# Kernel optimization log

Hardware: AMD Instinct MI355X
Metric: run time of the kernel (lower is better)

The kernel has to match this reference:

```python
import jax, jax.numpy as jnp
import numpy as np

D_MODEL = 1024
N_HEADS = 16
HEAD_DIM = D_MODEL // N_HEADS
D_FF = 4096
B, S = 2, 2048


def layer_norm(x, gamma, beta, eps=1e-5):
    mu = jnp.mean(x, axis=-1, keepdims=True)
    var = jnp.mean(jnp.square(x - mu), axis=-1, keepdims=True)
    return (x - mu) * jax.lax.rsqrt(var + eps) * gamma + beta


def setup_inputs() -> dict:
    key = jax.random.key(0)
    ks = jax.random.split(key, 8)
    s = 0.02
    return {
        "x": jax.random.normal(ks[0], (B, S, D_MODEL), dtype=jnp.float32),
        "qkv_w": jax.random.normal(ks[1], (D_MODEL, 3 * D_MODEL), dtype=jnp.float32) * s,
        "qkv_b": jnp.zeros((3 * D_MODEL,), jnp.float32),
        "out_w": jax.random.normal(ks[2], (D_MODEL, D_MODEL), dtype=jnp.float32) * s,
        "out_b": jnp.zeros((D_MODEL,), jnp.float32),
        "attn_ln_g": jnp.ones((D_MODEL,), jnp.float32),
        "attn_ln_b": jnp.zeros((D_MODEL,), jnp.float32),
        "norm1_g": jnp.ones((D_MODEL,), jnp.float32),
        "norm1_b": jnp.zeros((D_MODEL,), jnp.float32),
        "ff_ln_g": jnp.ones((D_MODEL,), jnp.float32),
        "ff_ln_b": jnp.zeros((D_MODEL,), jnp.float32),
        "w1": jax.random.normal(ks[3], (D_MODEL, D_FF), dtype=jnp.float32) * s,
        "b1": jnp.zeros((D_FF,), jnp.float32),
        "w2": jax.random.normal(ks[4], (D_FF, D_MODEL), dtype=jnp.float32) * s,
        "b2": jnp.zeros((D_MODEL,), jnp.float32),
        "norm2_g": jnp.ones((D_MODEL,), jnp.float32),
        "norm2_b": jnp.zeros((D_MODEL,), jnp.float32),
    }


def reference(x, qkv_w, qkv_b, out_w, out_b, attn_ln_g, attn_ln_b,
              norm1_g, norm1_b, ff_ln_g, ff_ln_b, w1, b1, w2, b2,
              norm2_g, norm2_b):
    # --- MultiHeadAttention (pre-LN inside the attn block) ---
    h = layer_norm(x, attn_ln_g, attn_ln_b)
    qkv = h @ qkv_w + qkv_b                       # [B,S,3D]
    qkv = qkv.reshape(B, S, 3, N_HEADS, HEAD_DIM)
    q = jnp.transpose(qkv[:, :, 0], (0, 2, 1, 3))  # [B,H,S,hd]
    k = jnp.transpose(qkv[:, :, 1], (0, 2, 1, 3))
    v = jnp.transpose(qkv[:, :, 2], (0, 2, 1, 3))
    scale = HEAD_DIM ** -0.5
    scores = jnp.einsum("bhqd,bhkd->bhqk", q, k) * scale  # [B,H,S,S]
    attn = jax.nn.softmax(scores, axis=-1)
    ctx = jnp.einsum("bhqk,bhkd->bhqd", attn, v)
    ctx = jnp.transpose(ctx, (0, 2, 1, 3)).reshape(B, S, D_MODEL)
    attn_out = ctx @ out_w + out_b

    # residual + post-LN
    x = layer_norm(x + attn_out, norm1_g, norm1_b)

    # --- FeedForward (pre-LN inside the FF block, GELU) ---
    h = layer_norm(x, ff_ln_g, ff_ln_b)
    ff = jax.nn.gelu(h @ w1 + b1, approximate=False) @ w2 + b2

    # residual + post-LN
    return layer_norm(x + ff, norm2_g, norm2_b)
```

## Files before the change

kernel.cpp:

```cpp
#include <hip/hip_runtime.h>
#include <hip/hip_bf16.h>

typedef __attribute__((ext_vector_type(4))) float f32x4;
typedef __attribute__((ext_vector_type(16))) float f32x16;
typedef __attribute__((ext_vector_type(8))) short s16x8;
typedef __attribute__((ext_vector_type(4))) short s16x4;

#define DM 1024
#define NH 16
#define NB 2
#define NS 2048
#define NTOK (NB*NS)

__device__ __forceinline__ float b2f(short u){
  union { unsigned int i; float f; } c; c.i = ((unsigned int)(unsigned short)u) << 16; return c.f;
}
__device__ __forceinline__ short f2b(float f){
  __hip_bfloat16 h = __float2bfloat16(f);
  return __builtin_bit_cast(short, h);
}
__device__ __forceinline__ void gload16(const void* g, void* l){
  __builtin_amdgcn_global_load_lds((const __attribute__((address_space(1))) void*)g,
                                   (__attribute__((address_space(3))) void*)l, 16, 0, 0);
}
__device__ __forceinline__ s16x4 tr16(const void* p){
  s16x4 r;
  asm volatile("ds_read_b64_tr_b16 %0, %1"
               : "=v"(r)
               : "v"((const __attribute__((address_space(3))) short*)p)
               : "memory");
  return r;
}

#define BARX { __builtin_amdgcn_sched_barrier(0); __builtin_amdgcn_s_barrier(); __builtin_amdgcn_sched_barrier(0); }
#define LGK  { asm volatile("s_waitcnt lgkmcnt(0)" ::: "memory"); __builtin_amdgcn_sched_barrier(0); }

template<int MIH>
__device__ __forceinline__ void rdA(s16x8 (&Af)[4][2], const short* Ab, int foff){
  #pragma unroll
  for (int m=0;m<4;m++)
    #pragma unroll
    for (int ks=0;ks<2;ks++)
      Af[m][ks] = *(const s16x8*)(Ab + (MIH*4+m)*1024 + ks*512 + foff);
}
template<int NIH>
__device__ __forceinline__ void rdB(s16x8 (&Bf)[4][2], const short* Bb, int foff){
  #pragma unroll
  for (int n=0;n<2;n++)
    #pragma unroll
    for (int ks=0;ks<2;ks++)
      Bf[NIH*2+n][ks] = *(const s16x8*)(Bb + (NIH*2+n)*1024 + ks*512 + foff);
}
template<int MIH,int NIH>
__device__ __forceinline__ void mmQ(f32x4 (&acc)[8][4], s16x8 (&Af)[4][2], s16x8 (&Bf)[4][2]){
  __builtin_amdgcn_s_setprio(1);
  #pragma unroll
  for (int m=0;m<4;m++)
    #pragma unroll
    for (int n=0;n<2;n++)
      #pragma unroll
      for (int ks=0;ks<2;ks++)
        acc[MIH*4+m][NIH*2+n] = __builtin_amdgcn_mfma_f32_16x16x32_bf16(
            Af[m][ks], Bf[NIH*2+n][ks], acc[MIH*4+m][NIH*2+n], 0,0,0);
  __builtin_amdgcn_s_setprio(0);
}

template<int GELU, int SPLITS>
__global__ __launch_bounds__(512,2) void gemm8p(
    const short* __restrict__ A, const short* __restrict__ Bt,
    const float* __restrict__ bias,
    short* __restrict__ C0, short* __restrict__ C1,
    short* __restrict__ C2, short* __restrict__ C3,
    int M, int N, int Ktot)
{
  __shared__ short Al[2*16384];
  __shared__ short Bl[2*16384];
  int tid = threadIdx.x, wid = tid>>6, lane = tid&63;
  int la = lane&15, lb = lane>>4;
  int z = blockIdx.z;
  const int Ksp = Ktot / SPLITS;
  short* C = (SPLITS==1) ? C0 : (z==0?C0 : z==1?C1 : z==2?C2 : C3);
  const short* Az  = A  + z*Ksp;
  const short* Btz = Bt + z*Ksp;
  int nbn = N>>8;
  int nwg = (M>>8)*nbn;
  int bid = (int)blockIdx.x;
  int sid = (bid&7)*(nwg>>3) + (bid>>3);
  int bm = sid / nbn, bn = sid % nbn;
  int wm2 = wid>>2, wn4 = wid&3;
  int bhalf = wn4>>1, bq4 = (wn4&1)*4;

  const short* aA0 = Az  + (size_t)(bm*256)*Ktot;
  const short* aA1 = Az  + (size_t)(bm*256+128)*Ktot;
  const short* bB0 = Btz + (size_t)(bn*256)*Ktot;
  const short* bB1 = Btz + (size_t)(bn*256+128)*Ktot;

  auto stG = [&](short* dstHalf, const short* srcRow0, int kt){
    #pragma unroll
    for (int c=0;c<2;c++){
      int s = c*8 + wid;
      int row = ((s>>1)<<4) + (lane>>2);
      int kk  = kt + ((s&1)<<5) + (((lane&3)<<3) ^ ((lane&32)>>1));
      gload16(srcRow0 + (size_t)row*Ktot + kk, dstHalf + s*512);
    }
  };

  int NJ = Ksp>>7;
  stG(&Al[0], aA0, 0);      stG(&Al[8192], aA1, 0);
  stG(&Bl[0], bB0, 0);      stG(&Bl[8192], bB1, 0);
  stG(&Bl[16384], bB0, 64); stG(&Bl[16384+8192], bB1, 64);
  asm volatile("s_waitcnt vmcnt(4)" ::: "memory");
  BARX;

  f32x4 acc[8][4] = {};
  s16x8 Af[4][2], Bf[4][2];
  int foff = la*32 + ((lb*8) ^ ((la&8)<<1));

  const short* Ab0c = &Al[wm2*8192];
  const short* Ab1c = &Al[16384 + wm2*8192];
  const short* Bb0c = &Bl[bhalf*8192 + bq4*1024];
  const short* Bb1c = &Bl[16384 + bhalf*8192 + bq4*1024];

  for (int j=0;j<NJ;j++){
    bool more = (j+1 < NJ);
    int ktA  = (2*j+1)*64;
    int ktN0 = (2*j+2)*64, ktN1 = (2*j+3)*64;
    rdA<0>(Af, Ab0c, foff); rdB<0>(Bf, Bb0c, foff);
    stG(&Al[16384], aA0, ktA);
    BARX; LGK; mmQ<0,0>(acc,Af,Bf); BARX;
    rdB<1>(Bf, Bb0c, foff);
    stG(&Al[16384+8192], aA1, ktA);
    BARX; LGK; mmQ<0,1>(acc,Af,Bf); BARX;
    rdA<1>(Af, Ab0c, foff);
    if (more) stG(&Bl[0], bB0, ktN0);
    BARX; LGK; mmQ<1,1>(acc,Af,Bf); BARX;
    if (more){ stG(&Bl[8192], bB1, ktN0);
               asm volatile("s_waitcnt vmcnt(4)" ::: "memory"); }
    else     { asm volatile("s_waitcnt vmcnt(0)" ::: "memory"); }
    BARX; mmQ<1,0>(acc,Af,Bf); BARX;
    rdA<0>(Af, Ab1c, foff); rdB<0>(Bf, Bb1c, foff);
    if (more) stG(&Al[0], aA0, ktN0);
    BARX; LGK; mmQ<0,0>(acc,Af,Bf); BARX;
    rdB<1>(Bf, Bb1c, foff);
    if (more) stG(&Al[8192], aA1, ktN0);
    BARX; LGK; mmQ<0,1>(acc,Af,Bf); BARX;
    rdA<1>(Af, Ab1c, foff);
    if (more) stG(&Bl[16384], bB0, ktN1);
    BARX; LGK; mmQ<1,1>(acc,Af,Bf); BARX;
    if (more){ stG(&Bl[16384+8192], bB1, ktN1);
               asm volatile("s_waitcnt vmcnt(4)" ::: "memory"); }
    else     { asm volatile("s_waitcnt vmcnt(0)" ::: "memory"); }
    BARX; mmQ<1,0>(acc,Af,Bf); BARX;
  }

  #pragma unroll
  for (int ni=0;ni<4;ni++){
    int col = bn*256 + wn4*64 + ni*16 + la;
    float bv = (SPLITS==1 || z==0) ? bias[col] : 0.0f;
    #pragma unroll
    for (int mi=0;mi<8;mi++){
      int row0 = bm*256 + wm2*128 + mi*16 + lb*4;
      #pragma unroll
      for (int j=0;j<4;j++){
        float v = acc[mi][ni][j] + bv;
        if (GELU) v = 0.5f*v*(1.0f + erff(v*0.70710678118f));
        C[(size_t)(row0+j)*N + col] = f2b(v);
      }
    }
  }
}

__global__ __launch_bounds__(512,1) void attn_fwd(const short* __restrict__ qkv, short* __restrict__ ctx)
{
  __shared__ short KlS[2*4096];
  __shared__ short VlS[2*4096];
  __shared__ float stats[8*32];
  char* Kl = (char*)KlS; char* Vl = (char*)VlS;
  int tid=threadIdx.x, w=tid>>6, lane=tid&63;
  int q5=lane&31, hi=lane>>5, la=lane&15, lb0=(lane>>4)&1;
  int qt=blockIdx.x, bh=blockIdx.y;
  int b=bh>>4, h=bh&15;
  int q0w = qt*256 + w*32;

  const short* qp = qkv + (size_t)(b*NS+q0w+q5)*3072 + h*64 + hi*8;
  s16x8 qf[4];
  #pragma unroll
  for (int ds=0; ds<4; ds++){
    s16x8 v = *(const s16x8*)(qp + ds*16);
    #pragma unroll
    for (int j=0;j<8;j++) v[j] = f2b(b2f(v[j])*0.125f);
    qf[ds]=v;
  }

  int krow = 8*w + (lane>>3);
  int kcolS = (((lane&7) ^ ((lane>>3)&7)) << 3);
  const short* Ksrc = qkv + (size_t)(b*NS+krow)*3072 + h*64 + 1024 + kcolS;
  int vk = 16*(w&3) + 8*hi + 4*lb0 + ((lane>>1)&3);
  int vd = 32*(w>>2) + 16*((lane>>3)&1) + 8*(lane&1);
  const short* Vsrc = qkv + (size_t)(b*NS+vk)*3072 + h*64 + 2048 + vd;

  int sw = (q5&7)<<4;
  int baseK = q5*128 + ((hi<<4) ^ (sw&16)) + (sw&96);
  int baseV = hi*512 + lb0*128 + la*8;

  f32x16 cacc0={}, cacc1={};
  float mrow=-1e30f, lrow=0.f;
  const size_t tstep = (size_t)64*3072;

  gload16(Ksrc, Kl + w*1024);
  gload16(Vsrc, Vl + w*1024);
  __syncthreads();
  int cur=0;

  for (int t=0;t<NS/64;t++){
    if (t+1 < NS/64){
      gload16(Ksrc + (size_t)(t+1)*tstep, Kl + (cur^1)*8192 + w*1024);
      gload16(Vsrc + (size_t)(t+1)*tstep, Vl + (cur^1)*8192 + w*1024);
    }
    const char* Kb = Kl + cur*8192;
    f32x16 s0={}, s1={};
    #pragma unroll
    for (int ds=0; ds<4; ds++){
      s16x8 k0 = *(const s16x8*)(Kb + (baseK ^ (ds<<5)));
      s16x8 k1 = *(const s16x8*)(Kb + 4096 + (baseK ^ (ds<<5)));
      s0 = __builtin_amdgcn_mfma_f32_32x32x16_bf16(k0, qf[ds], s0, 0,0,0);
      s1 = __builtin_amdgcn_mfma_f32_32x32x16_bf16(k1, qf[ds], s1, 0,0,0);
    }
    float pmax = s0[0];
    #pragma unroll
    for (int r=1;r<16;r++) pmax = fmaxf(pmax, s0[r]);
    #pragma unroll
    for (int r=0;r<16;r++) pmax = fmaxf(pmax, s1[r]);
    pmax = fmaxf(pmax, __shfl_xor(pmax, 32, 64));
    if (__any(pmax > mrow + 8.f)){
      float mnew = fmaxf(mrow, pmax);
      float corr = __expf(mrow - mnew);
      if (!hi) stats[w*32+q5] = corr;
      LGK;
      lrow *= corr; mrow = mnew;
      #pragma unroll
      for (int r=0;r<16;r++){
        float c = stats[w*32 + ((r&3)+8*(r>>2)+4*hi)];
        cacc0[r]*=c; cacc1[r]*=c;
      }
    }
    float rs = 0.f;
    #pragma unroll
    for (int r=0;r<16;r++){ float p=__expf(s0[r]-mrow); s0[r]=p; rs+=p; }
    #pragma unroll
    for (int r=0;r<16;r++){ float p=__expf(s1[r]-mrow); s1[r]=p; rs+=p; }
    rs += __shfl_xor(rs, 32, 64);
    lrow += rs;
    unsigned int D0[4][2], D1[4][2], R0[4][2], R1[4][2];
    #pragma unroll
    for (int bb=0;bb<4;bb++)
      #pragma unroll
      for (int hh=0;hh<2;hh++){
        D0[bb][hh] = (unsigned int)(unsigned short)f2b(s0[4*bb+2*hh]) |
                     ((unsigned int)(unsigned short)f2b(s0[4*bb+2*hh+1])<<16);
        D1[bb][hh] = (unsigned int)(unsigned short)f2b(s1[4*bb+2*hh]) |
                     ((unsigned int)(unsigned short)f2b(s1[4*bb+2*hh+1])<<16);
      }
    #pragma unroll
    for (int bb=0;bb<4;bb++)
      #pragma unroll
      for (int hh=0;hh<2;hh++){
        R0[bb][hh] = (unsigned int)__shfl_xor((int)D0[bb][hh], 32, 64);
        R1[bb][hh] = (unsigned int)__shfl_xor((int)D1[bb][hh], 32, 64);
      }
    union PA { unsigned int u[4]; s16x8 v; } pa[4];
    #pragma unroll
    for (int e=0;e<2;e++)
      #pragma unroll
      for (int hh=0;hh<2;hh++){
        pa[e].u[hh]     = hi ? R0[2*e+1][hh] : D0[2*e][hh];
        pa[e].u[2+hh]   = hi ? D0[2*e+1][hh] : R0[2*e][hh];
        pa[2+e].u[hh]   = hi ? R1[2*e+1][hh] : D1[2*e][hh];
        pa[2+e].u[2+hh] = hi ? D1[2*e+1][hh] : R1[2*e][hh];
      }
    const char* Vb = Vl + cur*8192;
    #pragma unroll
    for (int ks=0;ks<4;ks++){
      s16x4 t00 = tr16(Vb + ks*1024 +        0 + baseV);
      s16x4 t01 = tr16(Vb + ks*1024 +      256 + baseV);
      s16x4 t10 = tr16(Vb + ks*1024 + 4096     + baseV);
      s16x4 t11 = tr16(Vb + ks*1024 + 4096+256 + baseV);
      LGK;
      union { s16x4 hh[2]; s16x8 v; } u0, u1;
      u0.hh[0]=t00; u0.hh[1]=t01;
      u1.hh[0]=t10; u1.hh[1]=t11;
      cacc0 = __builtin_amdgcn_mfma_f32_32x32x16_bf16(pa[ks].v, u0.v, cacc0, 0,0,0);
      cacc1 = __builtin_amdgcn_mfma_f32_32x32x16_bf16(pa[ks].v, u1.v, cacc1, 0,0,0);
    }
    __syncthreads();
    cur ^= 1;
  }
  if (!hi) stats[w*32+q5] = 1.0f/lrow;
  LGK;
  #pragma unroll
  for (int r=0;r<16;r++){
    int q = (r&3)+8*(r>>2)+4*hi;
    float linv = stats[w*32+q];
    size_t row = (size_t)(b*NS + q0w + q)*DM + h*64;
    ctx[row + q5]      = f2b(cacc0[r]*linv);
    ctx[row + 32 + q5] = f2b(cacc1[r]*linv);
  }
}

__device__ __forceinline__ void wred2(float& s, float& ss){
  #pragma unroll
  for (int m=1;m<64;m<<=1){ s += __shfl_xor(s,m,64); ss += __shfl_xor(ss,m,64); }
}

__global__ __launch_bounds__(256) void ln_in(const float* __restrict__ x,
    const float* __restrict__ g, const float* __restrict__ be, short* __restrict__ out)
{
  int row=blockIdx.x, tid=threadIdx.x;
  __shared__ float r1[4], r2[4];
  float4 v = ((const float4*)(x + (size_t)row*DM))[tid];
  float s=v.x+v.y+v.z+v.w, ss=v.x*v.x+v.y*v.y+v.z*v.z+v.w*v.w;
  wred2(s,ss);
  if ((tid&63)==0){ r1[tid>>6]=s; r2[tid>>6]=ss; }
  __syncthreads();
  s=r1[0]+r1[1]+r1[2]+r1[3]; ss=r2[0]+r2[1]+r2[2]+r2[3];
  float mu=s*(1.f/DM);
  float rstd=rsqrtf(ss*(1.f/DM)-mu*mu+1e-5f);
  float4 gv=((const float4*)g)[tid], bv=((const float4*)be)[tid];
  s16x4 o;
  o[0]=f2b((v.x-mu)*rstd*gv.x+bv.x);
  o[1]=f2b((v.y-mu)*rstd*gv.y+bv.y);
  o[2]=f2b((v.z-mu)*rstd*gv.z+bv.z);
  o[3]=f2b((v.w-mu)*rstd*gv.w+bv.w);
  *(s16x4*)(out + (size_t)row*DM + tid*4) = o;
}

__global__ __launch_bounds__(256) void ln_chain(const float* __restrict__ x,
    const short* __restrict__ p0, const short* __restrict__ p1,
    const short* __restrict__ p2, const short* __restrict__ p3,
    const float* __restrict__ g1, const float* __restrict__ be1,
    const float* __restrict__ g2, const float* __restrict__ be2,
    float* __restrict__ x1, short* __restrict__ h2)
{
  int row=blockIdx.x, tid=threadIdx.x;
  __shared__ float r1[4], r2[4], r3[4], r4[4];
  size_t off = (size_t)row*DM + tid*4;
  float4 xv = ((const float4*)(x + (size_t)row*DM))[tid];
  s16x4 a0=*(const s16x4*)(p0+off), a1=*(const s16x4*)(p1+off);
  s16x4 a2=*(const s16x4*)(p2+off), a3=*(const s16x4*)(p3+off);
  float4 y;
  y.x = xv.x + b2f(a0[0])+b2f(a1[0])+b2f(a2[0])+b2f(a3[0]);
  y.y = xv.y + b2f(a0[1])+b2f(a1[1])+b2f(a2[1])+b2f(a3[1]);
  y.z = xv.z + b2f(a0[2])+b2f(a1[2])+b2f(a2[2])+b2f(a3[2]);
  y.w = xv.w + b2f(a0[3])+b2f(a1[3])+b2f(a2[3])+b2f(a3[3]);
  float s=y.x+y.y+y.z+y.w, ss=y.x*y.x+y.y*y.y+y.z*y.z+y.w*y.w;
  wred2(s,ss);
  if ((tid&63)==0){ r1[tid>>6]=s; r2[tid>>6]=ss; }
  __syncthreads();
  s=r1[0]+r1[1]+r1[2]+r1[3]; ss=r2[0]+r2[1]+r2[2]+r2[3];
  float mu=s*(1.f/DM);
  float rstd=rsqrtf(ss*(1.f/DM)-mu*mu+1e-5f);
  float4 g1v=((const float4*)g1)[tid], b1v=((const float4*)be1)[tid];
  float4 xo;
  xo.x=(y.x-mu)*rstd*g1v.x+b1v.x;
  xo.y=(y.y-mu)*rstd*g1v.y+b1v.y;
  xo.z=(y.z-mu)*rstd*g1v.z+b1v.z;
  xo.w=(y.w-mu)*rstd*g1v.w+b1v.w;
  ((float4*)(x1 + (size_t)row*DM))[tid] = xo;
  float s2=xo.x+xo.y+xo.z+xo.w, ss2=xo.x*xo.x+xo.y*xo.y+xo.z*xo.z+xo.w*xo.w;
  wred2(s2,ss2);
  if ((tid&63)==0){ r3[tid>>6]=s2; r4[tid>>6]=ss2; }
  __syncthreads();
  s2=r3[0]+r3[1]+r3[2]+r3[3]; ss2=r4[0]+r4[1]+r4[2]+r4[3];
  float mu2=s2*(1.f/DM);
  float rstd2=rsqrtf(ss2*(1.f/DM)-mu2*mu2+1e-5f);
  float4 g2v=((const float4*)g2)[tid], b2v=((const float4*)be2)[tid];
  s16x4 o;
  o[0]=f2b((xo.x-mu2)*rstd2*g2v.x+b2v.x);
  o[1]=f2b((xo.y-mu2)*rstd2*g2v.y+b2v.y);
  o[2]=f2b((xo.z-mu2)*rstd2*g2v.z+b2v.z);
  o[3]=f2b((xo.w-mu2)*rstd2*g2v.w+b2v.w);
  *(s16x4*)(h2 + off) = o;
}

__global__ __launch_bounds__(256) void ln_out_k(const float* __restrict__ x1,
    const short* __restrict__ p0, const short* __restrict__ p1,
    const short* __restrict__ p2, const short* __restrict__ p3,
    const float* __restrict__ g, const float* __restrict__ be, float* __restrict__ out)
{
  int row=blockIdx.x, tid=threadIdx.x;
  __shared__ float r1[4], r2[4];
  size_t off = (size_t)row*DM + tid*4;
  float4 xv = ((const float4*)(x1 + (size_t)row*DM))[tid];
  s16x4 a0=*(const s16x4*)(p0+off), a1=*(const s16x4*)(p1+off);
  s16x4 a2=*(const s16x4*)(p2+off), a3=*(const s16x4*)(p3+off);
  float4 y;
  y.x = xv.x + b2f(a0[0])+b2f(a1[0])+b2f(a2[0])+b2f(a3[0]);
  y.y = xv.y + b2f(a0[1])+b2f(a1[1])+b2f(a2[1])+b2f(a3[1]);
  y.z = xv.z + b2f(a0[2])+b2f(a1[2])+b2f(a2[2])+b2f(a3[2]);
  y.w = xv.w + b2f(a0[3])+b2f(a1[3])+b2f(a2[3])+b2f(a3[3]);
  float s=y.x+y.y+y.z+y.w, ss=y.x*y.x+y.y*y.y+y.z*y.z+y.w*y.w;
  wred2(s,ss);
  if ((tid&63)==0){ r1[tid>>6]=s; r2[tid>>6]=ss; }
  __syncthreads();
  s=r1[0]+r1[1]+r1[2]+r1[3]; ss=r2[0]+r2[1]+r2[2]+r2[3];
  float mu=s*(1.f/DM);
  float rstd=rsqrtf(ss*(1.f/DM)-mu*mu+1e-5f);
  float4 gv=((const float4*)g)[tid], bv=((const float4*)be)[tid];
  float4 o;
  o.x=(y.x-mu)*rstd*gv.x+bv.x;
  o.y=(y.y-mu)*rstd*gv.y+bv.y;
  o.z=(y.z-mu)*rstd*gv.z+bv.z;
  o.w=(y.w-mu)*rstd*gv.w+bv.w;
  ((float4*)(out + (size_t)row*DM))[tid] = o;
}

__global__ __launch_bounds__(256) void cast_t(const float* __restrict__ w, short* __restrict__ wt, int R, int C)
{
  __shared__ short t[64][65];
  int nbr = R>>6;
  int br = (int)blockIdx.x % nbr, bc = (int)blockIdx.x / nbr;
  int tid = threadIdx.x;
  #pragma unroll
  for (int i=0;i<4;i++){
    int c = i*256 + tid;
    int r = c>>4, c4 = (c&15)*4;
    float4 v = *(const float4*)(w + (size_t)(br*64 + r)*C + bc*64 + c4);
    t[r][c4+0]=f2b(v.x); t[r][c4+1]=f2b(v.y); t[r][c4+2]=f2b(v.z); t[r][c4+3]=f2b(v.w);
  }
  __syncthreads();
  #pragma unroll
  for (int i=0;i<4;i++){
    int c = i*256 + tid;
    int oc = c>>4, c4 = (c&15)*4;
    s16x4 p;
    p[0]=t[c4+0][oc]; p[1]=t[c4+1][oc]; p[2]=t[c4+2][oc]; p[3]=t[c4+3][oc];
    *(s16x4*)&wt[(size_t)(bc*64 + oc)*R + br*64 + c4] = p;
  }
}

extern "C" void kernel_launch(void* const* d_in, const int* in_sizes, int n_in,
                              void* d_out, int out_size, void* d_ws, size_t ws_size,
                              hipStream_t stream)
{
  const float* x      = (const float*)d_in[0];
  const float* qkv_w  = (const float*)d_in[1];
  const float* qkv_b  = (const float*)d_in[2];
  const float* out_w  = (const float*)d_in[3];
  const float* out_b  = (const float*)d_in[4];
  const float* aln_g  = (const float*)d_in[5];
  const float* aln_b  = (const float*)d_in[6];
  const float* n1_g   = (const float*)d_in[7];
  const float* n1_b   = (const float*)d_in[8];
  const float* fln_g  = (const float*)d_in[9];
  const float* fln_b  = (const float*)d_in[10];
  const float* w1     = (const float*)d_in[11];
  const float* b1     = (const float*)d_in[12];
  const float* w2     = (const float*)d_in[13];
  const float* b2     = (const float*)d_in[14];
  const float* n2_g   = (const float*)d_in[15];
  const float* n2_b   = (const float*)d_in[16];

  char* ws = (char*)d_ws;
  short* w2T   = (short*)(ws + 0);
  short* w1T   = (short*)(ws + 8388608);
  short* woutT = (short*)(ws + 16777216);
  short* wqkvT = (short*)(ws + 18874368);
  short* h1    = (short*)(ws + 25165824);
  short* qkv   = (short*)(ws + 33554432);
  short* ctx   = (short*)(ws + 58720256);
  float* x1    = (float*)(ws + 67108864);
  short* ff1   = (short*)(ws + 33554432);
  short* Po0 = (short*)(ws + 25165824);
  short* Po1 = (short*)(ws + 33554432);
  short* Po2 = (short*)(ws + 41943040);
  short* Po3 = (short*)(ws + 50331648);
  short* Pf0 = (short*)(ws + 8388608);
  short* Pf1 = (short*)(ws + 16777216);
  short* Pf2 = (short*)(ws + 25165824);
  short* Pf3 = (short*)(ws + 83886080);
  float* outp  = (float*)d_out;

  cast_t<<<dim3(16*48),256,0,stream>>>(qkv_w, wqkvT, 1024, 3072);
  cast_t<<<dim3(16*16),256,0,stream>>>(out_w, woutT, 1024, 1024);
  cast_t<<<dim3(16*64),256,0,stream>>>(w1,    w1T,   1024, 4096);
  cast_t<<<dim3(64*16),256,0,stream>>>(w2,    w2T,   4096, 1024);

  ln_in<<<NTOK,256,0,stream>>>(x, aln_g, aln_b, h1);
  gemm8p<0,1><<<dim3(192,1,1),512,0,stream>>>(h1, wqkvT, qkv_b, qkv,qkv,qkv,qkv, 4096,3072,1024);
  attn_fwd<<<dim3(8,32),512,0,stream>>>(qkv, ctx);
  gemm8p<0,4><<<dim3(64,1,4),512,0,stream>>>(ctx, woutT, out_b, Po0,Po1,Po2,Po3, 4096,1024,1024);
  ln_chain<<<NTOK,256,0,stream>>>(x, Po0,Po1,Po2,Po3, n1_g,n1_b, fln_g,fln_b, x1, h1);
  gemm8p<1,1><<<dim3(256,1,1),512,0,stream>>>(h1, w1T, b1, ff1,ff1,ff1,ff1, 4096,4096,1024);
  gemm8p<0,4><<<dim3(64,1,4),512,0,stream>>>(ff1, w2T, b2, Pf0,Pf1,Pf2,Pf3, 4096,1024,4096);
  ln_out_k<<<NTOK,256,0,stream>>>(x1, Pf0,Pf1,Pf2,Pf3, n2_g,n2_b, outp);
}
```

Measured before the change: 279.2 us.

## Halve attention block size to 4 waves, use exp2 softmax and truncating bf16 pack

The attention kernel now runs 256-thread blocks covering 128 queries each, with 2 blocks per CU and twice as many blocks. Each thread issues two K and two V global-to-LDS loads per tile to fill the same 64-key tile. Q is prescaled by log2(e) so the softmax can use exp2f instead of __expf. The P values are packed to bf16 by truncation rather than round-to-nearest. The grid change aims at better CU occupancy and more overlap across blocks, at the cost of more K/V reloads per query and slightly lower precision in P.

```diff
diff --git a/kernel.cpp b/kernel.cpp
--- a/kernel.cpp
+++ b/kernel.cpp
@@ -18,6 +18,11 @@
 __device__ __forceinline__ short f2b(float f){
   __hip_bfloat16 h = __float2bfloat16(f);
   return __builtin_bit_cast(short, h);
+}
+__device__ __forceinline__ unsigned pk2(float lo, float hi){
+  unsigned ul = __builtin_bit_cast(unsigned, lo);
+  unsigned uh = __builtin_bit_cast(unsigned, hi);
+  return (uh & 0xFFFF0000u) | (ul >> 16);
 }
 __device__ __forceinline__ void gload16(const void* g, void* l){
   __builtin_amdgcn_global_load_lds((const __attribute__((address_space(1))) void*)g,
@@ -170,34 +175,37 @@
   }
 }
 
-__global__ __launch_bounds__(512,1) void attn_fwd(const short* __restrict__ qkv, short* __restrict__ ctx)
+__global__ __launch_bounds__(256,2) void attn_fwd(const short* __restrict__ qkv, short* __restrict__ ctx)
 {
   __shared__ short KlS[2*4096];
   __shared__ short VlS[2*4096];
-  __shared__ float stats[8*32];
+  __shared__ float stats[4*32];
   char* Kl = (char*)KlS; char* Vl = (char*)VlS;
   int tid=threadIdx.x, w=tid>>6, lane=tid&63;
   int q5=lane&31, hi=lane>>5, la=lane&15, lb0=(lane>>4)&1;
   int qt=blockIdx.x, bh=blockIdx.y;
   int b=bh>>4, h=bh&15;
-  int q0w = qt*256 + w*32;
-
+  int q0w = qt*128 + w*32;
+
+  const float QSC = 0.125f * 1.44269504f;
   const short* qp = qkv + (size_t)(b*NS+q0w+q5)*3072 + h*64 + hi*8;
   s16x8 qf[4];
   #pragma unroll
   for (int ds=0; ds<4; ds++){
     s16x8 v = *(const s16x8*)(qp + ds*16);
     #pragma unroll
-    for (int j=0;j<8;j++) v[j] = f2b(b2f(v[j])*0.125f);
+    for (int j=0;j<8;j++) v[j] = f2b(b2f(v[j])*QSC);
     qf[ds]=v;
   }
 
   int krow = 8*w + (lane>>3);
   int kcolS = (((lane&7) ^ ((lane>>3)&7)) << 3);
-  const short* Ksrc = qkv + (size_t)(b*NS+krow)*3072 + h*64 + 1024 + kcolS;
-  int vk = 16*(w&3) + 8*hi + 4*lb0 + ((lane>>1)&3);
-  int vd = 32*(w>>2) + 16*((lane>>3)&1) + 8*(lane&1);
-  const short* Vsrc = qkv + (size_t)(b*NS+vk)*3072 + h*64 + 2048 + vd;
+  const short* KsrcA = qkv + (size_t)(b*NS+krow)*3072 + h*64 + 1024 + kcolS;
+  const short* KsrcB = KsrcA + (size_t)32*3072;
+  int vk = 16*w + 8*hi + 4*lb0 + ((lane>>1)&3);
+  int vd = 16*((lane>>3)&1) + 8*(lane&1);
+  const short* VsrcA = qkv + (size_t)(b*NS+vk)*3072 + h*64 + 2048 + vd;
+  const short* VsrcB = VsrcA + 32;
 
   int sw = (q5&7)<<4;
   int baseK = q5*128 + ((hi<<4) ^ (sw&16)) + (sw&96);
@@ -207,15 +215,20 @@
   float mrow=-1e30f, lrow=0.f;
   const size_t tstep = (size_t)64*3072;
 
-  gload16(Ksrc, Kl + w*1024);
-  gload16(Vsrc, Vl + w*1024);
+  gload16(KsrcA, Kl + w*1024);
+  gload16(KsrcB, Kl + w*1024 + 4096);
+  gload16(VsrcA, Vl + w*1024);
+  gload16(VsrcB, Vl + w*1024 + 4096);
   __syncthreads();
   int cur=0;
 
   for (int t=0;t<NS/64;t++){
     if (t+1 < NS/64){
-      gload16(Ksrc + (size_t)(t+1)*tstep, Kl + (cur^1)*8192 + w*1024);
-      gload16(Vsrc + (size_t)(t+1)*tstep, Vl + (cur^1)*8192 + w*1024);
+      size_t o = (size_t)(t+1)*tstep;
+      gload16(KsrcA + o, Kl + (cur^1)*8192 + w*1024);
+      gload16(KsrcB + o, Kl + (cur^1)*8192 + w*1024 + 4096);
+      gload16(VsrcA + o, Vl + (cur^1)*8192 + w*1024);
+      gload16(VsrcB + o, Vl + (cur^1)*8192 + w*1024 + 4096);
     }
     const char* Kb = Kl + cur*8192;
     f32x16 s0={}, s1={};
@@ -234,7 +247,7 @@
     pmax = fmaxf(pmax, __shfl_xor(pmax, 32, 64));
     if (__any(pmax > mrow + 8.f)){
       float mnew = fmaxf(mrow, pmax);
-      float corr = __expf(mrow - mnew);
+      float corr = exp2f(mrow - mnew);
       if (!hi) stats[w*32+q5] = corr;
       LGK;
       lrow *= corr; mrow = mnew;
@@ -246,9 +259,9 @@
     }
     float rs = 0.f;
     #pragma unroll
-    for (int r=0;r<16;r++){ float p=__expf(s0[r]-mrow); s0[r]=p; rs+=p; }
-    #pragma unroll
-    for (int r=0;r<16;r++){ float p=__expf(s1[r]-mrow); s1[r]=p; rs+=p; }
+    for (int r=0;r<16;r++){ float p=exp2f(s0[r]-mrow); s0[r]=p; rs+=p; }
+    #pragma unroll
+    for (int r=0;r<16;r++){ float p=exp2f(s1[r]-mrow); s1[r]=p; rs+=p; }
     rs += __shfl_xor(rs, 32, 64);
     lrow += rs;
     unsigned int D0[4][2], D1[4][2], R0[4][2], R1[4][2];
@@ -256,10 +269,8 @@
     for (int bb=0;bb<4;bb++)
       #pragma unroll
       for (int hh=0;hh<2;hh++){
-        D0[bb][hh] = (unsigned int)(unsigned short)f2b(s0[4*bb+2*hh]) |
-                     ((unsigned int)(unsigned short)f2b(s0[4*bb+2*hh+1])<<16);
-        D1[bb][hh] = (unsigned int)(unsigned short)f2b(s1[4*bb+2*hh]) |
-                     ((unsigned int)(unsigned short)f2b(s1[4*bb+2*hh+1])<<16);
+        D0[bb][hh] = pk2(s0[4*bb+2*hh], s0[4*bb+2*hh+1]);
+        D1[bb][hh] = pk2(s1[4*bb+2*hh], s1[4*bb+2*hh+1]);
       }
     #pragma unroll
     for (int bb=0;bb<4;bb++)
@@ -487,7 +498,7 @@
 
   ln_in<<<NTOK,256,0,stream>>>(x, aln_g, aln_b, h1);
   gemm8p<0,1><<<dim3(192,1,1),512,0,stream>>>(h1, wqkvT, qkv_b, qkv,qkv,qkv,qkv, 4096,3072,1024);
-  attn_fwd<<<dim3(8,32),512,0,stream>>>(qkv, ctx);
+  attn_fwd<<<dim3(16,32),256,0,stream>>>(qkv, ctx);
   gemm8p<0,4><<<dim3(64,1,4),512,0,stream>>>(ctx, woutT, out_b, Po0,Po1,Po2,Po3, 4096,1024,1024);
   ln_chain<<<NTOK,256,0,stream>>>(x, Po0,Po1,Po2,Po3, n1_g,n1_b, fln_g,fln_b, x1, h1);
   gemm8p<1,1><<<dim3(256,1,1),512,0,stream>>>(h1, w1T, b1, ff1,ff1,ff1,ff1, 4096,4096,1024);
```

Result: slower. 288.1 us (+3.2%).
